# Performance work log

Hardware: AMD Instinct MI355X
Metric: run time of the kernel (lower is better)

The kernel has to match this reference:

```python
import jax, jax.numpy as jnp
import numpy as np
from jax import lax

MAX_DEG = 10
BATCH = 4096
PER_DEG = 50000              # atoms per degree bucket
N_ATOMS = PER_DEG * (MAX_DEG + 1)
F = 128                      # n_atom_features == nb_filter
EPS = 1e-5


def setup_inputs() -> dict:
    key = jax.random.key(0)
    ks = jax.random.split(key, 8)
    atoms = jax.random.normal(ks[0], (N_ATOMS, F), jnp.float32)
    # atoms sorted by degree: degree d occupies rows [d*PER_DEG, (d+1)*PER_DEG)
    deg_slice = jnp.stack([jnp.arange(MAX_DEG + 1) * PER_DEG,
                           jnp.full((MAX_DEG + 1,), PER_DEG)], axis=1).astype(jnp.int32)
    membership = jax.random.randint(ks[1], (N_ATOMS,), 0, BATCH, dtype=jnp.int32)
    inp = {"atoms": atoms, "deg_slice": deg_slice, "membership": membership}
    for d in range(1, MAX_DEG + 1):
        inp[f"adj_{d}"] = jax.random.randint(jax.random.fold_in(key, d),
                                             (PER_DEG, d), 0, N_ATOMS, dtype=jnp.int32)
    inp["W"] = jax.random.normal(ks[2], (2 * MAX_DEG + 1, F, F), jnp.float32) * 0.05
    inp["b"] = jnp.zeros((2 * MAX_DEG + 1, F), jnp.float32)
    inp["gW"] = jax.random.normal(ks[3], (MAX_DEG + 1, F, F), jnp.float32) * 0.05
    inp["gb"] = jnp.zeros((MAX_DEG + 1, F), jnp.float32)
    inp["gamma"] = jnp.ones((F,), jnp.float32)
    inp["beta"] = jnp.zeros((F,), jnp.float32)
    return inp


def reference(atoms, deg_slice, membership,
              adj_1, adj_2, adj_3, adj_4, adj_5, adj_6, adj_7, adj_8, adj_9, adj_10,
              W, b, gW, gb, gamma, beta):
    adjs = [adj_1, adj_2, adj_3, adj_4, adj_5, adj_6, adj_7, adj_8, adj_9, adj_10]
    rel_outs = [None] * (MAX_DEG + 1)
    gat_outs = [None] * (MAX_DEG + 1)
    for d in range(1, MAX_DEG + 1):
        nbr_sum = jnp.take(atoms, adjs[d - 1], axis=0).sum(axis=1)  # (PER_DEG, F)
        self_atoms = lax.dynamic_slice_in_dim(atoms, deg_slice[d, 0], PER_DEG, axis=0)
        rel_outs[d] = (nbr_sum @ W[2 * (d - 1)] + b[2 * (d - 1)]
                       + self_atoms @ W[2 * (d - 1) + 1] + b[2 * (d - 1) + 1])
        gat_outs[d] = self_atoms @ gW[d - 1] + gb[d - 1]
    # degree 0 (min_deg == 0): self transform only
    self0 = lax.dynamic_slice_in_dim(atoms, deg_slice[0, 0], PER_DEG, axis=0)
    rel_outs[0] = self0 @ W[2 * MAX_DEG] + b[2 * MAX_DEG]
    gat_outs[0] = self0 @ gW[MAX_DEG] + gb[MAX_DEG]

    activated = jnp.concatenate(rel_outs, axis=0)     # (N_ATOMS, F), degree order == atom order
    gather_atoms = jnp.concatenate(gat_outs, axis=0)  # (N_ATOMS, F)
    # graph_gather: per-molecule sum (tf.dynamic_partition + reduce_sum == segment_sum)
    graph_feat = jax.ops.segment_sum(gather_atoms, membership, num_segments=BATCH)
    # activation is 'linear' (identity); layer-norm on atom features as in call()
    m = activated.mean(axis=-1, keepdims=True)
    std = jnp.sqrt(activated.var(axis=-1, keepdims=True) + EPS)
    normed = gamma * ((activated - m) / (std + EPS)) + beta
    return normed, graph_feat
```

## Files before the change

### kernel.cpp

```cpp
#include <hip/hip_runtime.h>
#include <hip/hip_bf16.h>

#define F_DIM   128
#define PER_DEG 50000
#define NDEG    11
#define MAXD    10
#define BATCH   4096
#define N_ATOMS (PER_DEG * NDEG)

#define BM     64
#define LDSN   136
#define BPD    ((PER_DEG + BM - 1) / BM)
#define WT_K   256
#define GWT_K  1440
#define LDST_L 264
#define WT_K_L 384

typedef __attribute__((ext_vector_type(4))) float f32x4;
typedef __attribute__((ext_vector_type(8))) short short8v;
typedef __attribute__((ext_vector_type(4))) short short4v;

struct AdjPtrs { const int* p[MAXD]; };

__device__ inline short bf16bits(float x) {
    __hip_bfloat16 h = __float2bfloat16(x);
    return __builtin_bit_cast(short, h);
}
__device__ inline float bf_lo(unsigned u) { return __builtin_bit_cast(float, u << 16); }
__device__ inline float bf_hi(unsigned u) { return __builtin_bit_cast(float, u & 0xFFFF0000u); }
__device__ inline float bf2f(short s) {
    return __builtin_bit_cast(float, ((unsigned)(unsigned short)s) << 16);
}
__device__ inline unsigned enc4_i8(float x0, float x1, float x2, float x3) {
    int q0 = (int)rintf(x0 * 16.0f), q1 = (int)rintf(x1 * 16.0f);
    int q2 = (int)rintf(x2 * 16.0f), q3 = (int)rintf(x3 * 16.0f);
    q0 = max(-127, min(127, q0)); q1 = max(-127, min(127, q1));
    q2 = max(-127, min(127, q2)); q3 = max(-127, min(127, q3));
    return (unsigned)(q0 & 255) | ((unsigned)(q1 & 255) << 8) |
           ((unsigned)(q2 & 255) << 16) | ((unsigned)(q3 & 255) << 24);
}
__device__ inline int sbyte(unsigned w, int k) {
    return (int)(w << (24 - 8 * k)) >> 24;
}

__global__ void prep_wt_main(const float* __restrict__ W, short* __restrict__ wt) {
    int idx = blockIdx.x * blockDim.x + threadIdx.x;
    const int total = NDEG * F_DIM * WT_K;
    if (idx >= total) return;
    int d   = idx / (F_DIM * WT_K);
    int rem = idx % (F_DIM * WT_K);
    int c   = rem / WT_K;
    int k   = rem % WT_K;
    float v;
    if (d == 0) {
        v = (k < 128) ? 0.0f : W[20 * 16384 + (k - 128) * F_DIM + c];
    } else {
        int wi = (k < 128) ? (2 * (d - 1)) : (2 * (d - 1) + 1);
        v = W[wi * 16384 + (k & 127) * F_DIM + c];
    }
    wt[idx] = bf16bits(v);
}

__global__ void prep_gwt(const float* __restrict__ gW, const float* __restrict__ gb,
                         short* __restrict__ gwt) {
    int idx = blockIdx.x * blockDim.x + threadIdx.x;
    const int total = F_DIM * GWT_K;
    if (idx >= total) return;
    int c = idx / GWT_K;
    int k = idx % GWT_K;
    float v = 0.0f;
    if (k < 1408) {
        int dd = k >> 7, f = k & 127;
        int gi = dd ? (dd - 1) : 10;
        v = gW[gi * 16384 + f * F_DIM + c];
    } else if (k < 1419) {
        int dd = k - 1408;
        int gi = dd ? (dd - 1) : 10;
        v = gb[gi * F_DIM + c];
    }
    gwt[idx] = bf16bits(v);
}

template<int WITH8>
__global__ void to_tables(const float* __restrict__ in, short* __restrict__ out,
                          unsigned char* __restrict__ out8) {
    const size_t n8 = (size_t)N_ATOMS * F_DIM / 8;
    size_t stride = (size_t)gridDim.x * blockDim.x;
    for (size_t k = (size_t)blockIdx.x * blockDim.x + threadIdx.x; k < n8; k += stride) {
        f32x4 a = __builtin_nontemporal_load((const f32x4*)in + 2 * k);
        f32x4 c = __builtin_nontemporal_load((const f32x4*)in + 2 * k + 1);
        short8v o = { bf16bits(a[0]), bf16bits(a[1]), bf16bits(a[2]), bf16bits(a[3]),
                      bf16bits(c[0]), bf16bits(c[1]), bf16bits(c[2]), bf16bits(c[3]) };
        ((short8v*)out)[k] = o;
        if (WITH8) {
            uint2 u;
            u.x = enc4_i8(a[0], a[1], a[2], a[3]);
            u.y = enc4_i8(c[0], c[1], c[2], c[3]);
            ((uint2*)out8)[k] = u;
        }
    }
}

__global__ void hist_kernel(const int* __restrict__ mem, int* __restrict__ hist2) {
    int i = blockIdx.x * blockDim.x + threadIdx.x;
    if (i >= N_ATOMS) return;
    atomicAdd(&hist2[mem[i] * NDEG + i / PER_DEG], 1);
}

__global__ void scan_offsets(const int* __restrict__ hist2,
                             int* __restrict__ off, int* __restrict__ cur) {
    __shared__ int lds[1024];
    const int tid = threadIdx.x;
    int h[4][NDEG];
    int tsum = 0;
    #pragma unroll
    for (int mi = 0; mi < 4; ++mi) {
        int m = tid * 4 + mi;
        #pragma unroll
        for (int dd = 0; dd < NDEG; ++dd) { h[mi][dd] = hist2[m * NDEG + dd]; tsum += h[mi][dd]; }
    }
    lds[tid] = tsum;
    __syncthreads();
    for (int ofs = 1; ofs < 1024; ofs <<= 1) {
        int v = (tid >= ofs) ? lds[tid - ofs] : 0;
        __syncthreads();
        lds[tid] += v;
        __syncthreads();
    }
    int run = lds[tid] - tsum;
    #pragma unroll
    for (int mi = 0; mi < 4; ++mi) {
        int m = tid * 4 + mi;
        #pragma unroll
        for (int dd = 0; dd < NDEG; ++dd) {
            int k = m * NDEG + dd;
            off[k] = run; cur[k] = run;
            run += h[mi][dd];
        }
    }
}

__global__ void scatter_kernel(const int* __restrict__ mem,
                               int* __restrict__ cur, int* __restrict__ idx) {
    int i = blockIdx.x * blockDim.x + threadIdx.x;
    if (i >= N_ATOMS) return;
    int pos = atomicAdd(&cur[mem[i] * NDEG + i / PER_DEG], 1);
    idx[pos] = i;
}

template<int I8>
__global__ __launch_bounds__(256, 4) void fused_deg(
    const short* __restrict__ abf,
    const unsigned char* __restrict__ ai8,
    AdjPtrs adj,
    const short* __restrict__ wt,
    const float* __restrict__ b,
    const float* __restrict__ gamma,
    const float* __restrict__ beta,
    float* __restrict__ outN)
{
    __shared__ short As[BM * LDSN];
    const int bid   = blockIdx.x;
    const int d     = bid / BPD;
    const int rb    = bid % BPD;
    const int rows0 = rb * BM;
    const int tid   = threadIdx.x;

    {
        const int rloc = tid >> 2;
        const int p    = tid & 3;
        const int grow = rows0 + rloc;
        short* basep = &As[rloc * LDSN + p * 32];
        if (I8) {
            int acci[32];
            #pragma unroll
            for (int e = 0; e < 32; ++e) acci[e] = 0;
            if (grow < PER_DEG && d > 0) {
                const int* ar = adj.p[d - 1] + (size_t)grow * d;
                int idxs[MAXD];
                #pragma unroll
                for (int j = 0; j < MAXD; ++j) idxs[j] = (j < d) ? ar[j] : 0;
                #pragma unroll
                for (int j = 0; j < MAXD; ++j) {
                    if (j < d) {
                        const uint4* rp = (const uint4*)(ai8 + (size_t)idxs[j] * F_DIM) + p * 2;
                        uint4 u0 = rp[0];
                        uint4 u1 = rp[1];
                        unsigned wds[8] = { u0.x, u0.y, u0.z, u0.w, u1.x, u1.y, u1.z, u1.w };
                        #pragma unroll
                        for (int dw = 0; dw < 8; ++dw) {
                            #pragma unroll
                            for (int k = 0; k < 4; ++k)
                                acci[dw * 4 + k] += sbyte(wds[dw], k);
                        }
                    }
                }
            }
            #pragma unroll
            for (int q = 0; q < 4; ++q) {
                short8v nb;
                #pragma unroll
                for (int e = 0; e < 8; ++e)
                    nb[e] = bf16bits((float)acci[q * 8 + e] * 0.0625f);
                *(short8v*)(basep + q * 8) = nb;
            }
        } else {
            float acc[32];
            #pragma unroll
            for (int e = 0; e < 32; ++e) acc[e] = 0.0f;
            if (grow < PER_DEG && d > 0) {
                const int* ar = adj.p[d - 1] + (size_t)grow * d;
                int idxs[MAXD];
                #pragma unroll
                for (int j = 0; j < MAXD; ++j) idxs[j] = (j < d) ? ar[j] : 0;
                #pragma unroll
                for (int j = 0; j < MAXD; ++j) {
                    if (j < d) {
                        const uint4* s = (const uint4*)(abf + (size_t)idxs[j] * F_DIM) + p * 4;
                        #pragma unroll
                        for (int q = 0; q < 4; ++q) {
                            uint4 u = s[q];
                            acc[q * 8 + 0] += bf_lo(u.x); acc[q * 8 + 1] += bf_hi(u.x);
                            acc[q * 8 + 2] += bf_lo(u.y); acc[q * 8 + 3] += bf_hi(u.y);
                            acc[q * 8 + 4] += bf_lo(u.z); acc[q * 8 + 5] += bf_hi(u.z);
                            acc[q * 8 + 6] += bf_lo(u.w); acc[q * 8 + 7] += bf_hi(u.w);
                        }
                    }
                }
            }
            #pragma unroll
            for (int q = 0; q < 4; ++q) {
                short8v nb = { bf16bits(acc[q * 8 + 0]), bf16bits(acc[q * 8 + 1]),
                               bf16bits(acc[q * 8 + 2]), bf16bits(acc[q * 8 + 3]),
                               bf16bits(acc[q * 8 + 4]), bf16bits(acc[q * 8 + 5]),
                               bf16bits(acc[q * 8 + 6]), bf16bits(acc[q * 8 + 7]) };
                *(short8v*)(basep + q * 8) = nb;
            }
        }
    }
    __syncthreads();

    const int w  = tid >> 6;
    const int l  = tid & 63;
    const int cg = l & 15;
    const int rg = l >> 4;

    short8v a[8];
    const short* arow = &As[(w * 16 + cg) * LDSN + rg * 8];
    #pragma unroll
    for (int s = 0; s < 4; ++s) a[s] = *(const short8v*)(arow + s * 32);
    int srow = d * PER_DEG + rows0 + w * 16 + cg;
    if (srow >= N_ATOMS) srow = N_ATOMS - 1;
    if (I8) {
        const unsigned char* sp8 = ai8 + (size_t)srow * F_DIM + rg * 8;
        #pragma unroll
        for (int s = 0; s < 4; ++s) {
            uint2 u = *(const uint2*)(sp8 + s * 32);
            short8v sv;
            #pragma unroll
            for (int e = 0; e < 8; ++e) {
                unsigned wd = (e < 4) ? u.x : u.y;
                sv[e] = bf16bits((float)sbyte(wd, e & 3) * 0.0625f);
            }
            a[4 + s] = sv;
        }
    } else {
        const short* sp = abf + (size_t)srow * F_DIM + rg * 8;
        #pragma unroll
        for (int s = 0; s < 4; ++s) a[4 + s] = *(const short8v*)(sp + s * 32);
    }

    const short* wtd = wt + (size_t)d * F_DIM * WT_K;
    f32x4 aA[8];
    #pragma unroll
    for (int n = 0; n < 8; ++n) aA[n] = 0.0f;
    #pragma unroll
    for (int s = 0; s < 8; ++s) {
        #pragma unroll
        for (int n = 0; n < 8; ++n) {
            short8v bv = *(const short8v*)(wtd + (n * 16 + cg) * WT_K + s * 32 + rg * 8);
            aA[n] = __builtin_amdgcn_mfma_f32_16x16x32_bf16(a[s], bv, aA[n], 0, 0, 0);
        }
    }

    float biasv[8], gam[8], bet[8];
    #pragma unroll
    for (int n = 0; n < 8; ++n) {
        int col = n * 16 + cg;
        biasv[n] = (d > 0) ? (b[(2 * d - 2) * F_DIM + col] + b[(2 * d - 1) * F_DIM + col])
                           : b[20 * F_DIM + col];
        gam[n] = gamma[col];
        bet[n] = beta[col];
    }
    const int valid = (PER_DEG - rows0 < BM) ? (PER_DEG - rows0) : BM;
    #pragma unroll
    for (int j = 0; j < 4; ++j) {
        const int rl = w * 16 + rg * 4 + j;
        float x[8];
        float s1 = 0.f, s2 = 0.f;
        #pragma unroll
        for (int n = 0; n < 8; ++n) {
            x[n] = aA[n][j] + biasv[n];
            s1 += x[n];
            s2 += x[n] * x[n];
        }
        #pragma unroll
        for (int m = 1; m < 16; m <<= 1) {
            s1 += __shfl_xor(s1, m);
            s2 += __shfl_xor(s2, m);
        }
        float mean = s1 * (1.0f / 128.0f);
        float var  = fmaxf(s2 * (1.0f / 128.0f) - mean * mean, 0.0f);
        float inv  = 1.0f / (sqrtf(var + 1e-5f) + 1e-5f);
        if (rl < valid) {
            float* op = outN + (size_t)(d * PER_DEG + rows0 + rl) * F_DIM;
            #pragma unroll
            for (int n = 0; n < 8; ++n)
                op[n * 16 + cg] = gam[n] * ((x[n] - mean) * inv) + bet[n];
        }
    }
}

__global__ __launch_bounds__(128) void mol_reduce(
    const short* __restrict__ abf, const int* __restrict__ idx,
    const int* __restrict__ off, const int* __restrict__ hist2,
    short* __restrict__ sums)
{
    const int key = blockIdx.x;
    const int m   = key / NDEG;
    const int dd  = key - m * NDEG;
    const int c   = threadIdx.x;
    const int base = off[key];
    const int n    = hist2[key];
    float acc = 0.0f;
    #pragma unroll 4
    for (int t = 0; t < n; ++t) {
        int id = idx[base + t];
        acc += bf2f(abf[(size_t)id * F_DIM + c]);
    }
    short* out = sums + (size_t)m * GWT_K;
    out[dd * F_DIM + c] = bf16bits(acc);
    if (c == 0) out[1408 + dd] = bf16bits((float)n);
    if (dd == 0 && c >= 11 && c < 32) out[1408 + c] = 0;
}

__global__ __launch_bounds__(256) void gat_gemm(
    const short* __restrict__ sums, const short* __restrict__ gwt,
    float* __restrict__ outG)
{
    const int rows0 = blockIdx.x * 64;
    const int tid = threadIdx.x;
    const int w = tid >> 6, l = tid & 63, cg = l & 15, rg = l >> 4;
    const short* ap = sums + (size_t)(rows0 + w * 16 + cg) * GWT_K + rg * 8;
    f32x4 acc[8];
    #pragma unroll
    for (int n = 0; n < 8; ++n) acc[n] = 0.0f;
    for (int ks = 0; ks < GWT_K / 32; ++ks) {
        short8v av = *(const short8v*)(ap + ks * 32);
        #pragma unroll
        for (int n = 0; n < 8; ++n) {
            short8v bv = *(const short8v*)(gwt + (size_t)(n * 16 + cg) * GWT_K + ks * 32 + rg * 8);
            acc[n] = __builtin_amdgcn_mfma_f32_16x16x32_bf16(av, bv, acc[n], 0, 0, 0);
        }
    }
    #pragma unroll
    for (int j = 0; j < 4; ++j) {
        int r = rows0 + w * 16 + rg * 4 + j;
        #pragma unroll
        for (int n = 0; n < 8; ++n)
            outG[(size_t)r * F_DIM + n * 16 + cg] = acc[n][j];
    }
}

__global__ void prep_wt_full(const float* __restrict__ W, const float* __restrict__ gW,
                             short* __restrict__ wt) {
    int idx = blockIdx.x * blockDim.x + threadIdx.x;
    const int total = NDEG * F_DIM * WT_K_L;
    if (idx >= total) return;
    int d   = idx / (F_DIM * WT_K_L);
    int rem = idx % (F_DIM * WT_K_L);
    int c   = rem / WT_K_L;
    int k   = rem % WT_K_L;
    float v;
    if (k < 256) {
        if (d == 0) v = (k < 128) ? 0.0f : W[20 * 16384 + (k - 128) * F_DIM + c];
        else {
            int wi = (k < 128) ? (2 * (d - 1)) : (2 * (d - 1) + 1);
            v = W[wi * 16384 + (k & 127) * F_DIM + c];
        }
    } else {
        int gi = (d == 0) ? 10 : (d - 1);
        v = gW[gi * 16384 + (k - 256) * F_DIM + c];
    }
    wt[idx] = bf16bits(v);
}

__global__ __launch_bounds__(256, 2) void fused_legacy(
    const float* __restrict__ atoms,
    const int* __restrict__ membership, AdjPtrs adj,
    const short* __restrict__ wt, const float* __restrict__ b,
    const float* __restrict__ gb, const float* __restrict__ gamma,
    const float* __restrict__ beta, float* __restrict__ outN, float* __restrict__ outG)
{
    __shared__ short As[BM * LDST_L];
    const int bid = blockIdx.x, d = bid / BPD, rb = bid % BPD;
    const int rows0 = rb * BM, tid = threadIdx.x;
    {
        const int rloc = tid >> 2, p = tid & 3;
        const int grow = rows0 + rloc;
        const bool rv = grow < PER_DEG;
        short* basep = &As[rloc * LDST_L + p * 32];
        f32x4 accn[8], selfv[8];
        #pragma unroll
        for (int q = 0; q < 8; ++q) { accn[q] = 0.0f; selfv[q] = 0.0f; }
        const f32x4* atomsv = (const f32x4*)atoms;
        if (rv) {
            if (d > 0) {
                const int* ar = adj.p[d - 1] + (size_t)grow * d;
                int idxs[MAXD];
                #pragma unroll
                for (int j = 0; j < MAXD; ++j) idxs[j] = (j < d) ? ar[j] : 0;
                #pragma unroll
                for (int j = 0; j < MAXD; ++j) if (j < d) {
                    const f32x4* s = atomsv + (size_t)idxs[j] * 32 + p * 8;
                    #pragma unroll
                    for (int q = 0; q < 8; ++q) accn[q] += s[q];
                }
            }
            const f32x4* s = atomsv + (size_t)(d * PER_DEG + grow) * 32 + p * 8;
            #pragma unroll
            for (int q = 0; q < 8; ++q) selfv[q] = s[q];
        }
        #pragma unroll
        for (int q = 0; q < 8; ++q) {
            short4v nb = { bf16bits(accn[q][0]), bf16bits(accn[q][1]),
                           bf16bits(accn[q][2]), bf16bits(accn[q][3]) };
            short4v sv = { bf16bits(selfv[q][0]), bf16bits(selfv[q][1]),
                           bf16bits(selfv[q][2]), bf16bits(selfv[q][3]) };
            *(short4v*)(basep + q * 4) = nb;
            *(short4v*)(basep + 128 + q * 4) = sv;
        }
    }
    __syncthreads();
    const int w = tid >> 6, l = tid & 63, cg = l & 15, rg = l >> 4;
    short8v a[8];
    const short* arow = &As[(w * 16 + cg) * LDST_L + rg * 8];
    #pragma unroll
    for (int s = 0; s < 8; ++s) a[s] = *(const short8v*)(arow + s * 32);
    const short* wtd = wt + (size_t)d * F_DIM * WT_K_L;
    f32x4 aA[8], aG[8];
    #pragma unroll
    for (int n = 0; n < 8; ++n) { aA[n] = 0.0f; aG[n] = 0.0f; }
    #pragma unroll
    for (int s = 0; s < 8; ++s) {
        #pragma unroll
        for (int n = 0; n < 8; ++n) {
            short8v bv = *(const short8v*)(wtd + (n * 16 + cg) * WT_K_L + s * 32 + rg * 8);
            aA[n] = __builtin_amdgcn_mfma_f32_16x16x32_bf16(a[s], bv, aA[n], 0, 0, 0);
        }
    }
    #pragma unroll
    for (int s = 0; s < 4; ++s) {
        #pragma unroll
        for (int n = 0; n < 8; ++n) {
            short8v bv = *(const short8v*)(wtd + (n * 16 + cg) * WT_K_L + 256 + s * 32 + rg * 8);
            aG[n] = __builtin_amdgcn_mfma_f32_16x16x32_bf16(a[4 + s], bv, aG[n], 0, 0, 0);
        }
    }
    const int gi = (d == 0) ? 10 : (d - 1);
    float biasv[8], gbv[8], gam[8], bet[8];
    #pragma unroll
    for (int n = 0; n < 8; ++n) {
        int col = n * 16 + cg;
        biasv[n] = (d > 0) ? (b[(2*d-2)*F_DIM+col] + b[(2*d-1)*F_DIM+col]) : b[20*F_DIM+col];
        gbv[n] = gb[gi * F_DIM + col];
        gam[n] = gamma[col]; bet[n] = beta[col];
    }
    const int valid = (PER_DEG - rows0 < BM) ? (PER_DEG - rows0) : BM;
    #pragma unroll
    for (int j = 0; j < 4; ++j) {
        const int rl = w * 16 + rg * 4 + j;
        float x[8], s1 = 0.f, s2 = 0.f;
        #pragma unroll
        for (int n = 0; n < 8; ++n) { x[n] = aA[n][j] + biasv[n]; s1 += x[n]; s2 += x[n]*x[n]; }
        #pragma unroll
        for (int m = 1; m < 16; m <<= 1) { s1 += __shfl_xor(s1, m); s2 += __shfl_xor(s2, m); }
        float mean = s1 * (1.0f/128.0f);
        float var  = fmaxf(s2 * (1.0f/128.0f) - mean*mean, 0.0f);
        float inv  = 1.0f / (sqrtf(var + 1e-5f) + 1e-5f);
        if (rl < valid) {
            const int growi = d * PER_DEG + rows0 + rl;
            float* op = outN + (size_t)growi * F_DIM;
            float* gp = outG + (size_t)membership[growi] * F_DIM;
            #pragma unroll
            for (int n = 0; n < 8; ++n) {
                int col = n * 16 + cg;
                op[col] = gam[n] * ((x[n] - mean) * inv) + bet[n];
                atomicAdd(&gp[col], aG[n][j] + gbv[n]);
            }
        }
    }
}

extern "C" void kernel_launch(void* const* d_in, const int* in_sizes, int n_in,
                              void* d_out, int out_size, void* d_ws, size_t ws_size,
                              hipStream_t stream) {
    const float* atoms      = (const float*)d_in[0];
    const int*   membership = (const int*)d_in[2];
    AdjPtrs adj;
    for (int i = 0; i < MAXD; ++i) adj.p[i] = (const int*)d_in[3 + i];
    const float* W     = (const float*)d_in[13];
    const float* b     = (const float*)d_in[14];
    const float* gW    = (const float*)d_in[15];
    const float* gb    = (const float*)d_in[16];
    const float* gamma = (const float*)d_in[17];
    const float* beta  = (const float*)d_in[18];

    float* outN = (float*)d_out;
    float* outG = outN + (size_t)N_ATOMS * F_DIM;

    auto al = [](size_t x) { return (x + 255) & ~(size_t)255; };
    const size_t sz_wt   = al((size_t)NDEG * F_DIM * WT_K * 2);
    const size_t sz_gwt  = al((size_t)F_DIM * GWT_K * 2);
    const size_t sz_h    = al((size_t)BATCH * NDEG * 4);
    const size_t sz_idx  = al((size_t)N_ATOMS * 4);
    const size_t sz_sums = al((size_t)BATCH * GWT_K * 2);
    const size_t sz_abf  = al((size_t)N_ATOMS * F_DIM * 2);
    const size_t sz_ai8  = (size_t)N_ATOMS * F_DIM;

    size_t o = 0;
    short* wt    = (short*)((char*)d_ws + o); o += sz_wt;
    short* gwt   = (short*)((char*)d_ws + o); o += sz_gwt;
    int*   hist2 = (int*)  ((char*)d_ws + o); o += sz_h;
    int*   offa  = (int*)  ((char*)d_ws + o); o += sz_h;
    int*   cura  = (int*)  ((char*)d_ws + o); o += sz_h;
    int*   idx   = (int*)  ((char*)d_ws + o); o += sz_idx;
    short* sums  = (short*)((char*)d_ws + o); o += sz_sums;
    short* abf   = (short*)((char*)d_ws + o); o += sz_abf;
    const size_t o_r5 = o;
    unsigned char* ai8 = (unsigned char*)((char*)d_ws + o); o += sz_ai8;

    if (ws_size >= o_r5) {
        const bool use_i8 = (ws_size >= o);
        prep_wt_main<<<(NDEG * F_DIM * WT_K + 255) / 256, 256, 0, stream>>>(W, wt);
        prep_gwt<<<(F_DIM * GWT_K + 255) / 256, 256, 0, stream>>>(gW, gb, gwt);
        hipMemsetAsync(hist2, 0, (size_t)BATCH * NDEG * 4, stream);
        if (use_i8)
            to_tables<1><<<2048, 256, 0, stream>>>(atoms, abf, ai8);
        else
            to_tables<0><<<2048, 256, 0, stream>>>(atoms, abf, nullptr);
        hist_kernel<<<(N_ATOMS + 255) / 256, 256, 0, stream>>>(membership, hist2);
        scan_offsets<<<1, 1024, 0, stream>>>(hist2, offa, cura);
        scatter_kernel<<<(N_ATOMS + 255) / 256, 256, 0, stream>>>(membership, cura, idx);
        if (use_i8)
            fused_deg<1><<<NDEG * BPD, 256, 0, stream>>>(abf, ai8, adj, wt, b,
                                                         gamma, beta, outN);
        else
            fused_deg<0><<<NDEG * BPD, 256, 0, stream>>>(abf, nullptr, adj, wt, b,
                                                         gamma, beta, outN);
        mol_reduce<<<BATCH * NDEG, 128, 0, stream>>>(abf, idx, offa, hist2, sums);
        gat_gemm<<<BATCH / 64, 256, 0, stream>>>(sums, gwt, outG);
    } else {
        short* lwt = (short*)d_ws;
        prep_wt_full<<<(NDEG * F_DIM * WT_K_L + 255) / 256, 256, 0, stream>>>(W, gW, lwt);
        hipMemsetAsync(outG, 0, (size_t)BATCH * F_DIM * 4, stream);
        fused_legacy<<<NDEG * BPD, 256, 0, stream>>>(atoms, membership, adj, lwt,
                                                     b, gb, gamma, beta, outN, outG);
    }
}
```

Before: 651.9 us.

## Drop bf16 atom table, prefetch int8 neighbor rows, interleave degree blocks

```diff
diff --git a/kernel.cpp b/kernel.cpp
--- a/kernel.cpp
+++ b/kernel.cpp
@@ -81,23 +81,16 @@
     gwt[idx] = bf16bits(v);
 }
 
-template<int WITH8>
-__global__ void to_tables(const float* __restrict__ in, short* __restrict__ out,
-                          unsigned char* __restrict__ out8) {
+__global__ void to_i8(const float* __restrict__ in, unsigned char* __restrict__ out8) {
     const size_t n8 = (size_t)N_ATOMS * F_DIM / 8;
     size_t stride = (size_t)gridDim.x * blockDim.x;
     for (size_t k = (size_t)blockIdx.x * blockDim.x + threadIdx.x; k < n8; k += stride) {
         f32x4 a = __builtin_nontemporal_load((const f32x4*)in + 2 * k);
         f32x4 c = __builtin_nontemporal_load((const f32x4*)in + 2 * k + 1);
-        short8v o = { bf16bits(a[0]), bf16bits(a[1]), bf16bits(a[2]), bf16bits(a[3]),
-                      bf16bits(c[0]), bf16bits(c[1]), bf16bits(c[2]), bf16bits(c[3]) };
-        ((short8v*)out)[k] = o;
-        if (WITH8) {
-            uint2 u;
-            u.x = enc4_i8(a[0], a[1], a[2], a[3]);
-            u.y = enc4_i8(c[0], c[1], c[2], c[3]);
-            ((uint2*)out8)[k] = u;
-        }
+        uint2 u;
+        u.x = enc4_i8(a[0], a[1], a[2], a[3]);
+        u.y = enc4_i8(c[0], c[1], c[2], c[3]);
+        ((uint2*)out8)[k] = u;
     }
 }
 
@@ -148,9 +141,7 @@
     idx[pos] = i;
 }
 
-template<int I8>
 __global__ __launch_bounds__(256, 4) void fused_deg(
-    const short* __restrict__ abf,
     const unsigned char* __restrict__ ai8,
     AdjPtrs adj,
     const short* __restrict__ wt,
@@ -161,8 +152,8 @@
 {
     __shared__ short As[BM * LDSN];
     const int bid   = blockIdx.x;
-    const int d     = bid / BPD;
-    const int rb    = bid % BPD;
+    const int d     = bid % NDEG;
+    const int rb    = bid / NDEG;
     const int rows0 = rb * BM;
     const int tid   = threadIdx.x;
 
@@ -171,71 +162,51 @@
         const int p    = tid & 3;
         const int grow = rows0 + rloc;
         short* basep = &As[rloc * LDSN + p * 32];
-        if (I8) {
-            int acci[32];
-            #pragma unroll
-            for (int e = 0; e < 32; ++e) acci[e] = 0;
-            if (grow < PER_DEG && d > 0) {
-                const int* ar = adj.p[d - 1] + (size_t)grow * d;
-                int idxs[MAXD];
-                #pragma unroll
-                for (int j = 0; j < MAXD; ++j) idxs[j] = (j < d) ? ar[j] : 0;
-                #pragma unroll
-                for (int j = 0; j < MAXD; ++j) {
-                    if (j < d) {
-                        const uint4* rp = (const uint4*)(ai8 + (size_t)idxs[j] * F_DIM) + p * 2;
-                        uint4 u0 = rp[0];
-                        uint4 u1 = rp[1];
-                        unsigned wds[8] = { u0.x, u0.y, u0.z, u0.w, u1.x, u1.y, u1.z, u1.w };
+        int acci[32];
+        #pragma unroll
+        for (int e = 0; e < 32; ++e) acci[e] = 0;
+        if (grow < PER_DEG && d > 0) {
+            const int* ar = adj.p[d - 1] + (size_t)grow * d;
+            int idxs[MAXD];
+            #pragma unroll
+            for (int j = 0; j < MAXD; ++j) idxs[j] = (j < d) ? ar[j] : 0;
+            uint4 b0x, b0y, b1x, b1y, b2x, b2y;
+            {
+                const uint4* r0 = (const uint4*)(ai8 + (size_t)idxs[0] * F_DIM) + p * 2;
+                b0x = r0[0]; b0y = r0[1];
+            }
+            if (d > 1) {
+                const uint4* r1 = (const uint4*)(ai8 + (size_t)idxs[1] * F_DIM) + p * 2;
+                b1x = r1[0]; b1y = r1[1];
+            }
+            #pragma unroll
+            for (int j = 0; j < MAXD; ++j) {
+                if (j < d) {
+                    if (j + 2 < d) {
+                        const uint4* rn =
+                            (const uint4*)(ai8 + (size_t)idxs[j + 2] * F_DIM) + p * 2;
+                        b2x = rn[0]; b2y = rn[1];
+                    }
+                    unsigned wds[8] = { b0x.x, b0x.y, b0x.z, b0x.w,
+                                        b0y.x, b0y.y, b0y.z, b0y.w };
+                    #pragma unroll
+                    for (int dw = 0; dw < 8; ++dw) {
                         #pragma unroll
-                        for (int dw = 0; dw < 8; ++dw) {
-                            #pragma unroll
-                            for (int k = 0; k < 4; ++k)
-                                acci[dw * 4 + k] += sbyte(wds[dw], k);
-                        }
+                        for (int k = 0; k < 4; ++k)
+                            acci[dw * 4 + k] += sbyte(wds[dw], k);
                     }
+                    b0x = b1x; b0y = b1y;
+                    b1x = b2x; b1y = b2y;
                 }
             }
-            #pragma unroll
-            for (int q = 0; q < 4; ++q) {
-                short8v nb;
-                #pragma unroll
-                for (int e = 0; e < 8; ++e)
-                    nb[e] = bf16bits((float)acci[q * 8 + e] * 0.0625f);
-                *(short8v*)(basep + q * 8) = nb;
-            }
-        } else {
-            float acc[32];
-            #pragma unroll
-            for (int e = 0; e < 32; ++e) acc[e] = 0.0f;
-            if (grow < PER_DEG && d > 0) {
-                const int* ar = adj.p[d - 1] + (size_t)grow * d;
-                int idxs[MAXD];
-                #pragma unroll
-                for (int j = 0; j < MAXD; ++j) idxs[j] = (j < d) ? ar[j] : 0;
-                #pragma unroll
-                for (int j = 0; j < MAXD; ++j) {
-                    if (j < d) {
-                        const uint4* s = (const uint4*)(abf + (size_t)idxs[j] * F_DIM) + p * 4;
-                        #pragma unroll
-                        for (int q = 0; q < 4; ++q) {
-                            uint4 u = s[q];
-                            acc[q * 8 + 0] += bf_lo(u.x); acc[q * 8 + 1] += bf_hi(u.x);
-                            acc[q * 8 + 2] += bf_lo(u.y); acc[q * 8 + 3] += bf_hi(u.y);
-                            acc[q * 8 + 4] += bf_lo(u.z); acc[q * 8 + 5] += bf_hi(u.z);
-                            acc[q * 8 + 6] += bf_lo(u.w); acc[q * 8 + 7] += bf_hi(u.w);
-                        }
-                    }
-                }
-            }
-            #pragma unroll
-            for (int q = 0; q < 4; ++q) {
-                short8v nb = { bf16bits(acc[q * 8 + 0]), bf16bits(acc[q * 8 + 1]),
-                               bf16bits(acc[q * 8 + 2]), bf16bits(acc[q * 8 + 3]),
-                               bf16bits(acc[q * 8 + 4]), bf16bits(acc[q * 8 + 5]),
-                               bf16bits(acc[q * 8 + 6]), bf16bits(acc[q * 8 + 7]) };
-                *(short8v*)(basep + q * 8) = nb;
-            }
+        }
+        #pragma unroll
+        for (int q = 0; q < 4; ++q) {
+            short8v nb;
+            #pragma unroll
+            for (int e = 0; e < 8; ++e)
+                nb[e] = bf16bits((float)acci[q * 8 + e] * 0.0625f);
+            *(short8v*)(basep + q * 8) = nb;
         }
     }
     __syncthreads();
@@ -251,7 +222,7 @@
     for (int s = 0; s < 4; ++s) a[s] = *(const short8v*)(arow + s * 32);
     int srow = d * PER_DEG + rows0 + w * 16 + cg;
     if (srow >= N_ATOMS) srow = N_ATOMS - 1;
-    if (I8) {
+    {
         const unsigned char* sp8 = ai8 + (size_t)srow * F_DIM + rg * 8;
         #pragma unroll
         for (int s = 0; s < 4; ++s) {
@@ -264,10 +235,6 @@
             }
             a[4 + s] = sv;
         }
-    } else {
-        const short* sp = abf + (size_t)srow * F_DIM + rg * 8;
-        #pragma unroll
-        for (int s = 0; s < 4; ++s) a[4 + s] = *(const short8v*)(sp + s * 32);
     }
 
     const short* wtd = wt + (size_t)d * F_DIM * WT_K;
@@ -322,7 +289,7 @@
 }
 
 __global__ __launch_bounds__(128) void mol_reduce(
-    const short* __restrict__ abf, const int* __restrict__ idx,
+    const float* __restrict__ atoms, const int* __restrict__ idx,
     const int* __restrict__ off, const int* __restrict__ hist2,
     short* __restrict__ sums)
 {
@@ -333,10 +300,18 @@
     const int base = off[key];
     const int n    = hist2[key];
     float acc = 0.0f;
-    #pragma unroll 4
-    for (int t = 0; t < n; ++t) {
-        int id = idx[base + t];
-        acc += bf2f(abf[(size_t)id * F_DIM + c]);
+    if (n > 0) {
+        int id0 = idx[base];
+        float vcur = atoms[(size_t)id0 * F_DIM + c];
+        for (int t = 0; t < n; ++t) {
+            float vnext = 0.0f;
+            if (t + 1 < n) {
+                int id1 = idx[base + t + 1];
+                vnext = atoms[(size_t)id1 * F_DIM + c];
+            }
+            acc += vcur;
+            vcur = vnext;
+        }
     }
     short* out = sums + (size_t)m * GWT_K;
     out[dd * F_DIM + c] = bf16bits(acc);
@@ -525,7 +500,6 @@
     const size_t sz_h    = al((size_t)BATCH * NDEG * 4);
     const size_t sz_idx  = al((size_t)N_ATOMS * 4);
     const size_t sz_sums = al((size_t)BATCH * GWT_K * 2);
-    const size_t sz_abf  = al((size_t)N_ATOMS * F_DIM * 2);
     const size_t sz_ai8  = (size_t)N_ATOMS * F_DIM;
 
     size_t o = 0;
@@ -536,29 +510,18 @@
     int*   cura  = (int*)  ((char*)d_ws + o); o += sz_h;
     int*   idx   = (int*)  ((char*)d_ws + o); o += sz_idx;
     short* sums  = (short*)((char*)d_ws + o); o += sz_sums;
-    short* abf   = (short*)((char*)d_ws + o); o += sz_abf;
-    const size_t o_r5 = o;
     unsigned char* ai8 = (unsigned char*)((char*)d_ws + o); o += sz_ai8;
 
-    if (ws_size >= o_r5) {
-        const bool use_i8 = (ws_size >= o);
+    if (ws_size >= o) {
         prep_wt_main<<<(NDEG * F_DIM * WT_K + 255) / 256, 256, 0, stream>>>(W, wt);
         prep_gwt<<<(F_DIM * GWT_K + 255) / 256, 256, 0, stream>>>(gW, gb, gwt);
         hipMemsetAsync(hist2, 0, (size_t)BATCH * NDEG * 4, stream);
-        if (use_i8)
-            to_tables<1><<<2048, 256, 0, stream>>>(atoms, abf, ai8);
-        else
-            to_tables<0><<<2048, 256, 0, stream>>>(atoms, abf, nullptr);
+        to_i8<<<2048, 256, 0, stream>>>(atoms, ai8);
         hist_kernel<<<(N_ATOMS + 255) / 256, 256, 0, stream>>>(membership, hist2);
         scan_offsets<<<1, 1024, 0, stream>>>(hist2, offa, cura);
         scatter_kernel<<<(N_ATOMS + 255) / 256, 256, 0, stream>>>(membership, cura, idx);
-        if (use_i8)
-            fused_deg<1><<<NDEG * BPD, 256, 0, stream>>>(abf, ai8, adj, wt, b,
-                                                         gamma, beta, outN);
-        else
-            fused_deg<0><<<NDEG * BPD, 256, 0, stream>>>(abf, nullptr, adj, wt, b,
-                                                         gamma, beta, outN);
-        mol_reduce<<<BATCH * NDEG, 128, 0, stream>>>(abf, idx, offa, hist2, sums);
+        fused_deg<<<NDEG * BPD, 256, 0, stream>>>(ai8, adj, wt, b, gamma, beta, outN);
+        mol_reduce<<<BATCH * NDEG, 128, 0, stream>>>(atoms, idx, offa, hist2, sums);
         gat_gemm<<<BATCH / 64, 256, 0, stream>>>(sums, gwt, outG);
     } else {
         short* lwt = (short*)d_ws;
```

New measurement: 634.7 us. 1.03x faster.
